# Performance work log

Measured on AMD Instinct MI355X. Metric: run time of the kernel, lower is better.

The kernel has to match this reference:

```python
import jax, jax.numpy as jnp
import numpy as np

H = 2048          # hidden_size
NH = 16           # num_heads
HD = H // NH      # head_dim = 128
B, S = 2, 2048


def setup_inputs() -> dict:
    key = jax.random.key(0)
    ks = jax.random.split(key, 9)
    sc_h = 1.0 / np.sqrt(H)
    x = jax.random.normal(ks[0], (B, S, H), dtype=jnp.float32)
    # torch nn.Linear weights are [out_features, in_features]
    Wq = jax.random.uniform(ks[1], (H, H), jnp.float32, -sc_h, sc_h)
    bq = jax.random.uniform(ks[2], (H,), jnp.float32, -sc_h, sc_h)
    Wk = jax.random.uniform(ks[3], (HD, H), jnp.float32, -sc_h, sc_h)
    bk = jax.random.uniform(ks[4], (HD,), jnp.float32, -sc_h, sc_h)
    Wv = jax.random.uniform(ks[5], (HD, H), jnp.float32, -sc_h, sc_h)
    bv = jax.random.uniform(ks[6], (HD,), jnp.float32, -sc_h, sc_h)
    Wo = jax.random.uniform(ks[7], (H, H), jnp.float32, -sc_h, sc_h)
    bo = jax.random.uniform(ks[8], (H,), jnp.float32, -sc_h, sc_h)
    return {"x": x, "Wq": Wq, "bq": bq, "Wk": Wk, "bk": bk,
            "Wv": Wv, "bv": bv, "Wo": Wo, "bo": bo}


def reference(x, Wq, bq, Wk, bk, Wv, bv, Wo, bo):
    b, s, _ = x.shape
    q = (jnp.einsum('bsh,oh->bso', x, Wq) + bq).reshape(b, s, NH, HD)
    q = q.transpose(0, 2, 1, 3)                      # [b, nh, s, hd]
    k = jnp.einsum('bsh,dh->bsd', x, Wk) + bk        # [b, s, hd] single KV head
    v = jnp.einsum('bsh,dh->bsd', x, Wv) + bv
    # shared-K attention scores: broadcast single K head across query heads
    attn = jnp.einsum('bnsd,btd->bnst', q, k) / jnp.sqrt(jnp.float32(HD))
    attn = jax.nn.softmax(attn, axis=-1)
    out = jnp.einsum('bnst,btd->bnsd', attn, v)      # [b, nh, s, hd]
    out = out.transpose(0, 2, 1, 3).reshape(b, s, H)
    return jnp.einsum('bsh,oh->bso', out, Wo) + bo
```

## Files before the change

### kernel.cpp

```cpp
#include <hip/hip_runtime.h>
#include <hip/hip_bf16.h>

typedef unsigned short u16;
typedef __bf16 bf16x8 __attribute__((ext_vector_type(8)));
typedef float f32x4 __attribute__((ext_vector_type(4)));

#define AS1 __attribute__((address_space(1)))
#define AS3 __attribute__((address_space(3)))

__device__ __forceinline__ u16 f2bf(float f) {
  unsigned u = __builtin_bit_cast(unsigned, f);
  u += 0x7FFFu + ((u >> 16) & 1u);
  return (u16)(u >> 16);
}

__device__ __forceinline__ void gload_lds16(const void* g, void* l) {
  __builtin_amdgcn_global_load_lds((AS1 void*)g, (AS3 void*)l, 16, 0, 0);
}

__global__ __launch_bounds__(256)
void cvt_all(const float* __restrict__ x,
             const float* __restrict__ Wq, const float* __restrict__ Wk,
             const float* __restrict__ Wv, const float* __restrict__ Wo,
             const float* __restrict__ bq, const float* __restrict__ bk,
             const float* __restrict__ bv,
             u16* __restrict__ xb, u16* __restrict__ wqkv, u16* __restrict__ wo,
             float* __restrict__ bias_a, float qs) {
  const long NX = 1048576, NQ = 524288, NK = 32768, NV = 32768, NO = 524288;
  const long NW = NX + NQ + NK + NV + NO;
  long i = (long)blockIdx.x * 256 + threadIdx.x;
  if (i >= NW) {
    int t = (int)(i - NW);
    if (t < 2048) bias_a[t] = bq[t] * qs;
    else if (t < 2176) bias_a[t] = bk[t - 2048];
    else if (t < 2304) bias_a[t] = bv[t - 2176];
    return;
  }
  const float* src;
  u16* dst;
  float s = 1.f;
  if (i < NX) { src = x + i * 8; dst = xb + i * 8; }
  else if (i < NX + NQ) { long j = i - NX; src = Wq + j * 8; dst = wqkv + j * 8; s = qs; }
  else if (i < NX + NQ + NK) { long j = i - NX - NQ; src = Wk + j * 8; dst = wqkv + 2048l * 2048 + j * 8; }
  else if (i < NX + NQ + NK + NV) { long j = i - NX - NQ - NK; src = Wv + j * 8; dst = wqkv + 2176l * 2048 + j * 8; }
  else { long j = i - NX - NQ - NK - NV; src = Wo + j * 8; dst = wo + j * 8; }
  float4 a = *(const float4*)src;
  float4 b = *(const float4*)(src + 4);
  u16 t[8] = {f2bf(a.x * s), f2bf(a.y * s), f2bf(a.z * s), f2bf(a.w * s),
              f2bf(b.x * s), f2bf(b.y * s), f2bf(b.z * s), f2bf(b.w * s)};
  *(uint4*)dst = *(const uint4*)t;
}

template<int MODE>
__global__ __launch_bounds__(256)
void gemm_bt(const u16* __restrict__ A, const u16* __restrict__ B,
             const float* __restrict__ bias, void* __restrict__ C0,
             void* __restrict__ C1, void* __restrict__ C2,
             int M, int N, int K, float scale)
{
  __shared__ u16 As[128 * 32];
  __shared__ u16 Bs[128 * 32];
  const int tid = threadIdx.x;
  const int wave = tid >> 6, lane = tid & 63;
  const int g = lane >> 4, r = lane & 15;
  const int wrow = (wave >> 1) * 64, wcol = (wave & 1) * 64;

  const int gx = gridDim.x;
  int lin = blockIdx.y * gx + blockIdx.x;
  const int cpx = (gx * gridDim.y) >> 3;
  lin = (lin & 7) * cpx + (lin >> 3);
  const long tM = (long)(lin / gx) * 128, tN = (long)(lin % gx) * 128;

  const int r0 = wave * 16 + (lane >> 2);
  const int c0 = (lane & 3) * 8;

  f32x4 acc[4][4] = {};
  char* As3 = (char*)As;
  char* Bs3 = (char*)Bs;

  for (int kt = 0; kt < K; kt += 32) {
    __syncthreads();
    const u16* gA = A + (tM + r0) * K + kt + c0;
    const u16* gB = B + (tN + r0) * K + kt + c0;
    gload_lds16(gA,                As3 + wave * 1024);
    gload_lds16(gA + (long)64 * K, As3 + 4096 + wave * 1024);
    gload_lds16(gB,                Bs3 + wave * 1024);
    gload_lds16(gB + (long)64 * K, Bs3 + 4096 + wave * 1024);
    __syncthreads();

    bf16x8 a[4], b[4];
#pragma unroll
    for (int m = 0; m < 4; m++)
      a[m] = *(const bf16x8*)(As + (wrow + m * 16 + r) * 32 + g * 8);
#pragma unroll
    for (int n = 0; n < 4; n++)
      b[n] = *(const bf16x8*)(Bs + (wcol + n * 16 + r) * 32 + g * 8);
#pragma unroll
    for (int m = 0; m < 4; m++)
#pragma unroll
      for (int n = 0; n < 4; n++)
        acc[m][n] = __builtin_amdgcn_mfma_f32_16x16x32_bf16(a[m], b[n], acc[m][n], 0, 0, 0);
  }

#pragma unroll
  for (int m = 0; m < 4; m++) {
    const long row0 = tM + wrow + m * 16 + g * 4;
#pragma unroll
    for (int n = 0; n < 4; n++) {
      const long col = tN + wcol + n * 16 + r;
      const float bb = bias[col];
      if (MODE == 0) {
#pragma unroll
        for (int q = 0; q < 4; q++)
          ((float*)C0)[(row0 + q) * N + col] = (acc[m][n][q] + bb) * scale;
      } else {
        u16 vals[4];
#pragma unroll
        for (int q = 0; q < 4; q++) vals[q] = f2bf(acc[m][n][q] + bb);
        if (col < 2048) {
#pragma unroll
          for (int q = 0; q < 4; q++)
            ((u16*)C0)[(row0 + q) * 2048 + col] = vals[q];
        } else if (col < 2176) {
#pragma unroll
          for (int q = 0; q < 4; q++)
            ((u16*)C1)[(row0 + q) * 128 + (col - 2048)] = vals[q];
        } else {
          const long b2 = row0 >> 11;
          const long t0r = row0 & 2047;
          const int tl = (int)(t0r & 63);
          const int rbase = tl & 15, blk = tl >> 4;
          u16* vp = (u16*)C2 + (b2 * 128 + (col - 2176)) * 2048 + (t0r >> 6) * 64;
#pragma unroll
          for (int q = 0; q < 4; q++)
            vp[(rbase + q) * 4 + blk] = vals[q];
        }
      }
    }
  }
}

__global__ __launch_bounds__(256, 2)
void attn_mqa12(const u16* __restrict__ Q, const u16* __restrict__ Kb,
                const u16* __restrict__ VT, u16* __restrict__ O)
{
  constexpr int S = 2048;
  const int bid = blockIdx.x;
  const int qt = bid & 15;
  const int head = (bid >> 4) & 15;
  const int b = bid >> 8;
  const int tid = threadIdx.x;
  const int wave = tid >> 6, lane = tid & 63;
  const int g = lane >> 4, r = lane & 15;

  __shared__ u16 Ks[2][64 * 128];
  __shared__ u16 VTs[2][128 * 64];
  __shared__ u16 Ps[4][16 * 64];

  bf16x8 qf[2][4];
#pragma unroll
  for (int qb = 0; qb < 2; qb++) {
    const u16* qp = Q + (long)(b * S + qt * 128 + qb * 64 + wave * 16 + r) * 2048
                      + head * 128 + g * 8;
#pragma unroll
    for (int ks = 0; ks < 4; ks++) qf[qb][ks] = *(const bf16x8*)(qp + ks * 32);
  }

  f32x4 oacc[2][8] = {};
  float lsum[2][4] = {};
  char* psb = (char*)Ps[wave];

  auto stageK = [&](int buf, int t0) {
    char* dst = (char*)Ks[buf];
#pragma unroll
    for (int p = 0; p < 4; p++) {
      int D = p * 4096 + wave * 1024 + lane * 16;
      int row = D >> 8;
      int col2 = (D & 255) ^ ((row & 7) << 4);
      gload_lds16(Kb + ((long)b * S + t0 + row) * 128 + (col2 >> 1), dst + D);
    }
  };
  auto stageV = [&](int buf, int t0) {
    char* dst = (char*)VTs[buf];
#pragma unroll
    for (int p = 0; p < 4; p++) {
      int D = p * 4096 + wave * 1024 + lane * 16;
      int row = D >> 7;
      int colb = (D & 127) ^ ((row & 7) << 4);
      gload_lds16(VT + ((long)b * 128 + row) * 2048 + t0 + (colb >> 1), dst + D);
    }
  };

  stageK(0, 0);
  stageV(0, 0);
  __syncthreads();

  for (int t0 = 0; t0 < S; t0 += 64) {
    const int cur = (t0 >> 6) & 1;
    const bool nxt = (t0 + 64) < S;

    if (nxt) { stageK(cur ^ 1, t0 + 64); stageV(cur ^ 1, t0 + 64); }

    char* Ks3 = (char*)Ks[cur];
    f32x4 st[2][4] = {};
    __builtin_amdgcn_s_setprio(1);
#pragma unroll
    for (int ks = 0; ks < 4; ks++) {
#pragma unroll
      for (int nf = 0; nf < 4; nf++) {
        const int trow = nf * 16 + r;
        const int col2 = (ks * 64 + g * 16) ^ ((trow & 7) << 4);
        bf16x8 kf = *(const bf16x8*)(Ks3 + trow * 256 + col2);
        st[0][nf] = __builtin_amdgcn_mfma_f32_16x16x32_bf16(qf[0][ks], kf, st[0][nf], 0, 0, 0);
        st[1][nf] = __builtin_amdgcn_mfma_f32_16x16x32_bf16(qf[1][ks], kf, st[1][nf], 0, 0, 0);
      }
    }
    __builtin_amdgcn_s_setprio(0);

    char* Vs3 = (char*)VTs[cur];
    bf16x8 vreg[2][8];
#pragma unroll
    for (int qb = 0; qb < 2; qb++) {
#pragma unroll
      for (int q = 0; q < 4; q++) {
        const int prow = g * 4 + q;
        u16 pk[4];
#pragma unroll
        for (int nf = 0; nf < 4; nf++) {
          float p = __builtin_amdgcn_exp2f(st[qb][nf][q]);
          lsum[qb][q] += p;
          pk[nf] = __builtin_bit_cast(u16, (__bf16)p);
        }
        *(ushort4*)(psb + prow * 128 + ((r * 8) ^ ((prow & 7) << 4))) =
            *(const ushort4*)pk;
      }
      __builtin_amdgcn_s_setprio(1);
#pragma unroll
      for (int ks = 0; ks < 2; ks++) {
        bf16x8 pf = *(const bf16x8*)(psb + r * 128 +
                                     ((ks * 64 + g * 16) ^ ((r & 7) << 4)));
#pragma unroll
        for (int dn = 0; dn < 8; dn++) {
          if (qb == 0) {
            const int d = dn * 16 + r;
            vreg[ks][dn] = *(const bf16x8*)(Vs3 + d * 128 +
                                            ((ks * 64 + g * 16) ^ ((d & 7) << 4)));
          }
          oacc[qb][dn] = __builtin_amdgcn_mfma_f32_16x16x32_bf16(pf, vreg[ks][dn],
                                                                 oacc[qb][dn], 0, 0, 0);
        }
      }
      __builtin_amdgcn_s_setprio(0);
    }

    __syncthreads();
  }

#pragma unroll
  for (int off = 1; off < 16; off <<= 1)
#pragma unroll
    for (int qb = 0; qb < 2; qb++)
#pragma unroll
      for (int q = 0; q < 4; q++)
        lsum[qb][q] += __shfl_xor(lsum[qb][q], off);

#pragma unroll
  for (int qb = 0; qb < 2; qb++) {
#pragma unroll
    for (int q = 0; q < 4; q++) {
      const float inv = 1.f / lsum[qb][q];
      const long orow = (long)(b * S + qt * 128 + qb * 64 + wave * 16 + g * 4 + q);
#pragma unroll
      for (int dn = 0; dn < 8; dn++)
        O[orow * 2048 + head * 128 + dn * 16 + r] = f2bf(oacc[qb][dn][q] * inv);
    }
  }
}

extern "C" void kernel_launch(void* const* d_in, const int* in_sizes, int n_in,
                              void* d_out, int out_size, void* d_ws, size_t ws_size,
                              hipStream_t stream) {
  const float* x  = (const float*)d_in[0];
  const float* Wq = (const float*)d_in[1];
  const float* bq = (const float*)d_in[2];
  const float* Wk = (const float*)d_in[3];
  const float* bk = (const float*)d_in[4];
  const float* Wv = (const float*)d_in[5];
  const float* bv = (const float*)d_in[6];
  const float* Wo = (const float*)d_in[7];
  const float* bo = (const float*)d_in[8];
  float* out = (float*)d_out;

  char* ws = (char*)d_ws;
  u16* x_bf     = (u16*)(ws + (0ul  << 20));
  u16* q_bf     = (u16*)(ws + (16ul << 20));
  u16* wqkv_bf  = (u16*)(ws + (32ul << 20));
  u16* wo_bf    = (u16*)(ws + (42ul << 20));
  u16* k_bf     = (u16*)(ws + (50ul << 20));
  u16* vt_bf    = (u16*)(ws + (51ul << 20));
  u16* attn_bf  = (u16*)(ws + (52ul << 20));
  float* bias_a = (float*)(ws + (68ul << 20));

  const float QS = 0.12751744f;

  cvt_all<<<8457, 256, 0, stream>>>(x, Wq, Wk, Wv, Wo, bq, bk, bv,
                                    x_bf, wqkv_bf, wo_bf, bias_a, QS);

  gemm_bt<3><<<dim3(18, 32), 256, 0, stream>>>(
      x_bf, wqkv_bf, bias_a, q_bf, k_bf, vt_bf, 4096, 2304, 2048, 1.0f);
  attn_mqa12<<<512, 256, 0, stream>>>(q_bf, k_bf, vt_bf, attn_bf);
  gemm_bt<0><<<dim3(16, 32), 256, 0, stream>>>(
      attn_bf, wo_bf, bo, out, nullptr, nullptr, 4096, 2048, 2048, 1.0f);
}
```

Baseline: 209.8 us.

## Double GEMM K-tile to 64 and XOR-swizzle LDS layout

The bf16 GEMM now stages a 128x64 K-slice of A and B per iteration instead of 128x32, which halves the number of barrier pairs per K loop. The LDS tiles use an XOR swizzle on the column index by row to avoid bank conflicts on the 16-byte fragment reads. LDS use per block doubles to 32KB, which may reduce occupancy.

```diff
diff --git a/kernel.cpp b/kernel.cpp
--- a/kernel.cpp
+++ b/kernel.cpp
@@ -58,8 +58,8 @@
              void* __restrict__ C1, void* __restrict__ C2,
              int M, int N, int K, float scale)
 {
-  __shared__ u16 As[128 * 32];
-  __shared__ u16 Bs[128 * 32];
+  __shared__ u16 As[128 * 64];
+  __shared__ u16 Bs[128 * 64];
   const int tid = threadIdx.x;
   const int wave = tid >> 6, lane = tid & 63;
   const int g = lane >> 4, r = lane & 15;
@@ -71,35 +71,43 @@
   lin = (lin & 7) * cpx + (lin >> 3);
   const long tM = (long)(lin / gx) * 128, tN = (long)(lin % gx) * 128;
 
-  const int r0 = wave * 16 + (lane >> 2);
-  const int c0 = (lane & 3) * 8;
+  const int srow = (tid * 16) >> 7;
+  const int scol = (tid & 7) * 8;
 
   f32x4 acc[4][4] = {};
   char* As3 = (char*)As;
   char* Bs3 = (char*)Bs;
 
-  for (int kt = 0; kt < K; kt += 32) {
+  for (int kt = 0; kt < K; kt += 64) {
     __syncthreads();
-    const u16* gA = A + (tM + r0) * K + kt + c0;
-    const u16* gB = B + (tN + r0) * K + kt + c0;
-    gload_lds16(gA,                As3 + wave * 1024);
-    gload_lds16(gA + (long)64 * K, As3 + 4096 + wave * 1024);
-    gload_lds16(gB,                Bs3 + wave * 1024);
-    gload_lds16(gB + (long)64 * K, Bs3 + 4096 + wave * 1024);
+#pragma unroll
+    for (int p = 0; p < 4; p++) {
+      const int row = p * 32 + srow;
+      const int sc = scol ^ ((row & 7) << 3);
+      gload_lds16(A + (tM + row) * K + kt + sc, As3 + p * 4096 + tid * 16);
+      gload_lds16(B + (tN + row) * K + kt + sc, Bs3 + p * 4096 + tid * 16);
+    }
     __syncthreads();
 
-    bf16x8 a[4], b[4];
-#pragma unroll
-    for (int m = 0; m < 4; m++)
-      a[m] = *(const bf16x8*)(As + (wrow + m * 16 + r) * 32 + g * 8);
-#pragma unroll
-    for (int n = 0; n < 4; n++)
-      b[n] = *(const bf16x8*)(Bs + (wcol + n * 16 + r) * 32 + g * 8);
-#pragma unroll
-    for (int m = 0; m < 4; m++)
-#pragma unroll
-      for (int n = 0; n < 4; n++)
-        acc[m][n] = __builtin_amdgcn_mfma_f32_16x16x32_bf16(a[m], b[n], acc[m][n], 0, 0, 0);
+#pragma unroll
+    for (int kk = 0; kk < 2; kk++) {
+      bf16x8 a[4], b[4];
+#pragma unroll
+      for (int m = 0; m < 4; m++) {
+        const int ra = wrow + m * 16 + r;
+        a[m] = *(const bf16x8*)(As + ra * 64 + ((kk * 32 + g * 8) ^ ((ra & 7) << 3)));
+      }
+#pragma unroll
+      for (int n = 0; n < 4; n++) {
+        const int rb = wcol + n * 16 + r;
+        b[n] = *(const bf16x8*)(Bs + rb * 64 + ((kk * 32 + g * 8) ^ ((rb & 7) << 3)));
+      }
+#pragma unroll
+      for (int m = 0; m < 4; m++)
+#pragma unroll
+        for (int n = 0; n < 4; n++)
+          acc[m][n] = __builtin_amdgcn_mfma_f32_16x16x32_bf16(a[m], b[n], acc[m][n], 0, 0, 0);
+    }
   }
 
 #pragma unroll
```

Result: faster. 190.5 us (-9.2%).
